# Optimization experiments

Hardware: AMD Instinct MI355X
Metric: run time of the kernel (lower is better)

Reference implementation:

```python
import jax, jax.numpy as jnp
import numpy as np

B, P = 16, 1024
D_TIME, NUM_MODS = 8, 22
DIM_S = NUM_MODS + D_TIME + 1  # 31
PHI_W, N_HEADS, DP = 32, 4, 32
PSI_W, PSI_L, RHO_W = 64, 64, 64
SQRT_DP = float(np.sqrt(DP))


def setup_inputs() -> dict:
    key = jax.random.key(0)
    ks = jax.random.split(key, 16)
    rn = lambda k, shape: jax.random.normal(k, shape, jnp.float32) * 0.05
    return dict(
        times=jax.random.uniform(ks[0], (B, P), jnp.float32) * 48.0,
        values=jax.random.normal(ks[1], (B, P), jnp.float32),
        measurements=jax.random.randint(ks[2], (B, P), 0, NUM_MODS + 1),
        non_pad_mask=jnp.ones((B, P, 1), jnp.float32),
        W_psi1=rn(ks[3], (DIM_S, PSI_W)), b_psi1=jnp.zeros((PSI_W,), jnp.float32),
        W_psi2=rn(ks[4], (PSI_W, PSI_L)), b_psi2=jnp.zeros((PSI_L,), jnp.float32),
        W_key=rn(ks[5], (DIM_S + PSI_L, N_HEADS * DP)), b_key=jnp.zeros((N_HEADS * DP,), jnp.float32),
        query=rn(ks[6], (N_HEADS, DP)),
        W_phi1=rn(ks[7], (DIM_S, PHI_W)), b_phi1=jnp.zeros((PHI_W,), jnp.float32),
        W_phi2=rn(ks[8], (PHI_W, PHI_W)), b_phi2=jnp.zeros((PHI_W,), jnp.float32),
        W_rho1=rn(ks[9], (N_HEADS * PHI_W, RHO_W)), b_rho1=jnp.zeros((RHO_W,), jnp.float32),
        W_rho2=rn(ks[10], (RHO_W, RHO_W)), b_rho2=jnp.zeros((RHO_W,), jnp.float32),
    )


def _temporal_enc(times):
    i = np.arange(D_TIME)
    pos_vec = jnp.asarray(10000.0 ** (2.0 * (i // 2) / D_TIME), jnp.float32)
    ang = times[:, :, None] / pos_vec  # [B,P,d_time]
    return jnp.where(jnp.asarray(i % 2 == 0), jnp.sin(ang), jnp.cos(ang))


def reference(times, values, measurements, non_pad_mask,
              W_psi1, b_psi1, W_psi2, b_psi2, W_key, b_key, query,
              W_phi1, b_phi1, W_phi2, b_phi2, W_rho1, b_rho1, W_rho2, b_rho2):
    m = non_pad_mask  # [B,P,1]
    te = _temporal_enc(times)
    oh = jax.nn.one_hot(measurements, NUM_MODS + 1, dtype=jnp.float32)[:, :, 1:]
    x = jnp.concatenate([te, values[:, :, None], oh], axis=-1)  # [B,P,dim_s]

    # CumulativeSetAttentionLayer: psi MLP -> cumulative mean -> keys . query
    psi = jax.nn.relu(jax.nn.relu(x @ W_psi1 + b_psi1) @ W_psi2 + b_psi2)  # [B,P,psi_l]
    cum = jnp.cumsum(psi * m, axis=1) / jnp.cumsum(m, axis=1)
    keys = (jnp.concatenate([x, cum], axis=-1) @ W_key + b_key).reshape(B, P, N_HEADS, DP)
    pre = jnp.einsum('bpmd,md->bpm', keys, query) / SQRT_DP  # [B,P,m]

    # phi MLP
    phi = jax.nn.relu(jax.nn.relu(x @ W_phi1 + b_phi1) @ W_phi2 + b_phi2) * m  # [B,P,phi_w]

    # cumulative softmax weighting (online path)
    cmax = jax.lax.cummax(pre, axis=1)  # [B,P,m], running max for stability
    D = jnp.exp(pre[:, None, :, :] - cmax[:, :, None, :])  # [B,P,Q,m]
    causal = jnp.arange(P)[:, None] >= jnp.arange(P)[None, :]  # keep Q <= P
    D = D * causal[None, :, :, None]
    E = D.sum(axis=2)  # [B,P,m]
    agg = jnp.einsum('bpqm,bqd->bpmd', D, phi) / E[:, :, :, None]
    agg = (agg * m[:, :, :, None]).reshape(B, P, N_HEADS * PHI_W)

    # rho MLP (return_sequences)
    out = jax.nn.relu(jax.nn.relu(agg @ W_rho1 + b_rho1) @ W_rho2 + b_rho2) * m
    return out
```

## Files before the change

### kernel.cpp

```cpp
#include <hip/hip_runtime.h>
#include <hip/hip_bf16.h>

#define B_ 16
#define P_ 1024
#define T_ (B_*P_)
#define CH_ 32
#define CL_ (P_/CH_)

constexpr int OFF_A     = 16;
constexpr int OFF_WPSI1 = 400;
constexpr int OFF_BPSI1 = OFF_WPSI1 + 1984;
constexpr int OFF_WPSI2 = OFF_BPSI1 + 64;
constexpr int OFF_BPSI2 = OFF_WPSI2 + 4096;
constexpr int OFF_WPHI1 = OFF_BPSI2 + 64;
constexpr int OFF_BPHI1 = OFF_WPHI1 + 992;
constexpr int OFF_WPHI2 = OFF_BPHI1 + 32;
constexpr int OFF_BPHI2 = OFF_WPHI2 + 1024;
constexpr int OFF_WRHO1 = OFF_BPHI2 + 32;
constexpr int OFF_BRHO1 = OFF_WRHO1 + 8192;
constexpr int OFF_WRHO2 = OFF_BRHO1 + 64;
constexpr int OFF_BRHO2 = OFF_WRHO2 + 4096;
constexpr int OFF_PHI   = OFF_BRHO2 + 64;
constexpr int OFF_Z     = OFF_PHI   + T_*32;
constexpr int OFF_PREX  = OFF_Z     + T_*4;
constexpr int OFF_EXPW  = OFF_PREX  + T_*4;
constexpr int OFF_CE    = OFF_EXPW  + T_*4;
constexpr int OFF_CS    = OFF_CE    + 2048;

static __device__ __forceinline__ bool detect_f32(const void* mask_raw) {
  return ((*(const unsigned*)mask_raw) & 0xFFFFu) == 0u;
}
static __device__ __forceinline__ float ld_any(const void* src, int i, bool isf32) {
  if (isf32) return ((const float*)src)[i];
  return __bfloat162float(((const __hip_bfloat16*)src)[i]);
}
static __device__ __forceinline__ float bfbits(unsigned u) {
  union { unsigned q; float f; } x; x.q = u << 16; return x.f;
}

__global__ __launch_bounds__(256) void s01_prep(
    float* __restrict__ ws, const void* mask,
    const void* Wpsi1, const void* bpsi1, const void* Wpsi2, const void* bpsi2,
    const void* Wkey,  const void* bkey,  const void* query,
    const void* Wphi1, const void* bphi1, const void* Wphi2, const void* bphi2) {
  const bool isf32 = detect_f32(mask);
  if (blockIdx.x < 2) {
    const int gid = blockIdx.x * 256 + threadIdx.x;
    if (gid >= 384) return;
    const float inv_s = 0.17677669529663687f;
    const int h = gid & 3;
    const int j = gid >> 2;
    float s = 0.f;
    if (j < 95) {
      for (int d = 0; d < 32; ++d)
        s += ld_any(Wkey, j * 128 + h * 32 + d, isf32) * ld_any(query, h * 32 + d, isf32);
    } else {
      for (int d = 0; d < 32; ++d)
        s += ld_any(bkey, h * 32 + d, isf32) * ld_any(query, h * 32 + d, isf32);
    }
    ws[OFF_A + gid] = s * inv_s;
    return;
  }
  const int g  = (blockIdx.x - 2) * 256 + threadIdx.x;
  const int gs = (gridDim.x - 2) * 256;
  auto st = [&](int off, const void* src, int n) {
    for (int i = g; i < n; i += gs) ws[off + i] = ld_any(src, i, isf32);
  };
  st(OFF_WPSI1, Wpsi1, 1984); st(OFF_BPSI1, bpsi1, 64);
  st(OFF_WPSI2, Wpsi2, 4096); st(OFF_BPSI2, bpsi2, 64);
  st(OFF_WPHI1, Wphi1, 992);  st(OFF_BPHI1, bphi1, 32);
  st(OFF_WPHI2, Wphi2, 1024); st(OFF_BPHI2, bphi2, 32);
}

__global__ __launch_bounds__(1024) void k1_token(float* __restrict__ ws,
                                                 const int* __restrict__ measp,
                                                 const void* __restrict__ times,
                                                 const void* __restrict__ values,
                                                 const void* __restrict__ mask) {
  __shared__ float sWS[8288];
  __shared__ float sh1[32][64];
  __shared__ float sg1[32][32];
  constexpr int LW1 = 0, LB1 = 1984, LW2 = 2048, LB2 = 6144;
  constexpr int LP1 = 6208, LQ1 = 7200, LP2 = 7232, LQ2 = 8256;
  const bool isf32 = detect_f32(mask);
  const int tid = threadIdx.x;
  const int wv  = __builtin_amdgcn_readfirstlane(tid >> 6);
  const int j   = tid & 63;
  const int ta  = blockIdx.x * 32 + wv * 2;
  const int tb  = ta + 1;

  const float tva = ld_any(times, ta, isf32),  tvb = ld_any(times, tb, isf32);
  const float vva = ld_any(values, ta, isf32), vvb = ld_any(values, tb, isf32);
  const float mva = ld_any(mask, ta, isf32),   mvb = ld_any(mask, tb, isf32);
  const int   mea = measp[ta],                 meb = measp[tb];

  {
    const float4* src = (const float4*)(ws + OFF_WPSI1);
    float4* dst = (float4*)sWS;
    for (int i = tid; i < 2072; i += 1024) dst[i] = src[i];
  }

  const float sea = (mea > 0) ? 1.f : 0.f;
  const float seb = (meb > 0) ? 1.f : 0.f;
  const int   mra = (mea > 0) ? (8 + mea) : 0;
  const int   mrb = (meb > 0) ? (8 + meb) : 0;

  float xa[9], xb[9];
  const float posv[4] = {1.f, 10.f, 100.f, 1000.f};
  #pragma unroll
  for (int k = 0; k < 4; ++k) {
    float s, c;
    __sincosf(tva / posv[k], &s, &c); xa[2*k] = s; xa[2*k+1] = c;
    __sincosf(tvb / posv[k], &s, &c); xb[2*k] = s; xb[2*k+1] = c;
  }
  xa[8] = vva; xb[8] = vvb;
  __syncthreads();

  float h1a = sWS[LB1 + j], h1b = h1a;
  #pragma unroll
  for (int i = 0; i < 9; ++i) {
    const float w = sWS[LW1 + i * 64 + j];
    h1a = fmaf(xa[i], w, h1a);
    h1b = fmaf(xb[i], w, h1b);
  }
  h1a = fmaf(sea, sWS[LW1 + mra * 64 + j], h1a);
  h1b = fmaf(seb, sWS[LW1 + mrb * 64 + j], h1b);
  sh1[wv * 2 + 0][j] = fmaxf(h1a, 0.f);
  sh1[wv * 2 + 1][j] = fmaxf(h1b, 0.f);

  if (j < 32) {
    float g1a = sWS[LQ1 + j], g1b = g1a;
    #pragma unroll
    for (int i = 0; i < 9; ++i) {
      const float w = sWS[LP1 + i * 32 + j];
      g1a = fmaf(xa[i], w, g1a);
      g1b = fmaf(xb[i], w, g1b);
    }
    g1a = fmaf(sea, sWS[LP1 + mra * 32 + j], g1a);
    g1b = fmaf(seb, sWS[LP1 + mrb * 32 + j], g1b);
    sg1[wv * 2 + 0][j] = fmaxf(g1a, 0.f);
    sg1[wv * 2 + 1][j] = fmaxf(g1b, 0.f);
  }
  __syncthreads();

  float h2a = sWS[LB2 + j], h2b = h2a;
  #pragma unroll 8
  for (int i = 0; i < 64; ++i) {
    const float w = sWS[LW2 + i * 64 + j];
    h2a = fmaf(sh1[wv * 2 + 0][i], w, h2a);
    h2b = fmaf(sh1[wv * 2 + 1][i], w, h2b);
  }
  const float qa = fmaxf(h2a, 0.f) * mva;
  const float qb = fmaxf(h2b, 0.f) * mvb;

  const float4 a2 = *(const float4*)(ws + OFF_A + (31 + j) * 4);
  float z0a = qa * a2.x, z1a = qa * a2.y, z2a = qa * a2.z, z3a = qa * a2.w;
  float z0b = qb * a2.x, z1b = qb * a2.y, z2b = qb * a2.z, z3b = qb * a2.w;
  #pragma unroll
  for (int off = 32; off; off >>= 1) {
    z0a += __shfl_xor(z0a, off, 64); z1a += __shfl_xor(z1a, off, 64);
    z2a += __shfl_xor(z2a, off, 64); z3a += __shfl_xor(z3a, off, 64);
    z0b += __shfl_xor(z0b, off, 64); z1b += __shfl_xor(z1b, off, 64);
    z2b += __shfl_xor(z2b, off, 64); z3b += __shfl_xor(z3b, off, 64);
  }
  if (j == 0) {
    float4 va; va.x = z0a; va.y = z1a; va.z = z2a; va.w = z3a;
    float4 vb; vb.x = z0b; vb.y = z1b; vb.z = z2b; vb.w = z3b;
    *(float4*)(ws + OFF_Z + (size_t)ta * 4) = va;
    *(float4*)(ws + OFF_Z + (size_t)tb * 4) = vb;
  }

  if (j < 32) {
    float g2a = sWS[LQ2 + j], g2b = g2a;
    #pragma unroll 8
    for (int i = 0; i < 32; ++i) {
      const float w = sWS[LP2 + i * 32 + j];
      g2a = fmaf(sg1[wv * 2 + 0][i], w, g2a);
      g2b = fmaf(sg1[wv * 2 + 1][i], w, g2b);
    }
    ws[OFF_PHI + (size_t)ta * 32 + j] = fmaxf(g2a, 0.f) * mva;
    ws[OFF_PHI + (size_t)tb * 32 + j] = fmaxf(g2b, 0.f) * mvb;
  } else if (j < 40) {
    const bool sec = j >= 36;
    const int h = (j - 32) & 3;
    const float sel  = sec ? seb : sea;
    const int   mrow = sec ? mrb : mra;
    const int   t    = sec ? tb : ta;
    float pr = ws[OFF_A + 380 + h];
    #pragma unroll
    for (int i = 0; i < 9; ++i) {
      const float xi = sec ? xb[i] : xa[i];
      pr = fmaf(xi, ws[OFF_A + i * 4 + h], pr);
    }
    pr = fmaf(sel, ws[OFF_A + mrow * 4 + h], pr);
    ws[OFF_PREX + (size_t)t * 4 + h] = pr;
  }
}

__global__ __launch_bounds__(256) void k2_scanz(float* __restrict__ ws,
                                                const void* __restrict__ mask) {
  const int b    = blockIdx.x;
  const int tid  = threadIdx.x;
  const int lane = tid & 63;
  const int wv   = tid >> 6;
  const bool isf32 = detect_f32(mask);
  __shared__ float swt[4][5];
  __shared__ float smx[4][4];

  const float* zB = ws + OFF_Z + (size_t)b * P_ * 4;
  const int p0 = tid * 4;

  float lc[4], l0[4], l1[4], l2[4], l3[4];
  float c = 0.f, z0 = 0.f, z1 = 0.f, z2 = 0.f, z3 = 0.f;
  const float4* z4 = (const float4*)(zB + (size_t)p0 * 4);
  #pragma unroll
  for (int i = 0; i < 4; ++i) {
    const float4 zv = z4[i];
    c  += ld_any(mask, b * P_ + p0 + i, isf32);
    z0 += zv.x; z1 += zv.y; z2 += zv.z; z3 += zv.w;
    lc[i] = c; l0[i] = z0; l1[i] = z1; l2[i] = z2; l3[i] = z3;
  }

  float rc = c, r0 = z0, r1 = z1, r2 = z2, r3 = z3;
  #pragma unroll
  for (int off = 1; off < 64; off <<= 1) {
    const float uc = __shfl_up(rc, off, 64);
    const float u0 = __shfl_up(r0, off, 64);
    const float u1 = __shfl_up(r1, off, 64);
    const float u2 = __shfl_up(r2, off, 64);
    const float u3 = __shfl_up(r3, off, 64);
    if (lane >= off) { rc += uc; r0 += u0; r1 += u1; r2 += u2; r3 += u3; }
  }
  if (lane == 63) {
    swt[wv][0] = rc; swt[wv][1] = r0; swt[wv][2] = r1; swt[wv][3] = r2; swt[wv][4] = r3;
  }
  __syncthreads();
  #pragma unroll
  for (int w2 = 0; w2 < 3; ++w2) {
    if (wv > w2) {
      rc += swt[w2][0]; r0 += swt[w2][1]; r1 += swt[w2][2];
      r2 += swt[w2][3]; r3 += swt[w2][4];
    }
  }
  const float ec = rc - c, e0 = r0 - z0, e1 = r1 - z1, e2 = r2 - z2, e3 = r3 - z3;

  const float* px = ws + OFF_PREX + (size_t)b * P_ * 4;
  const float4* px4 = (const float4*)(px + (size_t)p0 * 4);
  float pre[4][4];
  float mx0 = -1e30f, mx1 = -1e30f, mx2 = -1e30f, mx3 = -1e30f;
  #pragma unroll
  for (int i = 0; i < 4; ++i) {
    const float inv = 1.f / (ec + lc[i]);
    const float4 pv = px4[i];
    pre[i][0] = pv.x + (e0 + l0[i]) * inv;
    pre[i][1] = pv.y + (e1 + l1[i]) * inv;
    pre[i][2] = pv.z + (e2 + l2[i]) * inv;
    pre[i][3] = pv.w + (e3 + l3[i]) * inv;
    mx0 = fmaxf(mx0, pre[i][0]); mx1 = fmaxf(mx1, pre[i][1]);
    mx2 = fmaxf(mx2, pre[i][2]); mx3 = fmaxf(mx3, pre[i][3]);
  }

  #pragma unroll
  for (int off = 32; off; off >>= 1) {
    mx0 = fmaxf(mx0, __shfl_xor(mx0, off, 64));
    mx1 = fmaxf(mx1, __shfl_xor(mx1, off, 64));
    mx2 = fmaxf(mx2, __shfl_xor(mx2, off, 64));
    mx3 = fmaxf(mx3, __shfl_xor(mx3, off, 64));
  }
  if (lane == 0) { smx[wv][0] = mx0; smx[wv][1] = mx1; smx[wv][2] = mx2; smx[wv][3] = mx3; }
  __syncthreads();
  const float M0 = fmaxf(fmaxf(smx[0][0], smx[1][0]), fmaxf(smx[2][0], smx[3][0]));
  const float M1 = fmaxf(fmaxf(smx[0][1], smx[1][1]), fmaxf(smx[2][1], smx[3][1]));
  const float M2 = fmaxf(fmaxf(smx[0][2], smx[1][2]), fmaxf(smx[2][2], smx[3][2]));
  const float M3 = fmaxf(fmaxf(smx[0][3], smx[1][3]), fmaxf(smx[2][3], smx[3][3]));

  float* eB = ws + OFF_EXPW + (size_t)b * P_ * 4;
  float4* e4 = (float4*)(eB + (size_t)p0 * 4);
  #pragma unroll
  for (int i = 0; i < 4; ++i) {
    float4 ev;
    ev.x = __expf(pre[i][0] - M0);
    ev.y = __expf(pre[i][1] - M1);
    ev.z = __expf(pre[i][2] - M2);
    ev.w = __expf(pre[i][3] - M3);
    e4[i] = ev;
  }
}

__global__ __launch_bounds__(128) void k4a_sums(float* __restrict__ ws) {
  const int ch = blockIdx.x, b = blockIdx.y;
  const int h = threadIdx.x >> 5, d = threadIdx.x & 31;
  const float* eB   = ws + OFF_EXPW + (size_t)b * P_ * 4;
  const float* phiB = ws + OFF_PHI  + (size_t)b * P_ * 32;

  float E = 0.f, S = 0.f;
  const int pbeg = ch * CL_;
  #pragma unroll 4
  for (int p = pbeg; p < pbeg + CL_; ++p) {
    const float e  = eB[p * 4 + h];
    const float ph = phiB[p * 32 + d];
    E += e;
    S = fmaf(e, ph, S);
  }
  const int base = (b * CH_ + ch) * 4 + h;
  if (d == 0) ws[OFF_CE + base] = E;
  ws[OFF_CS + base * 32 + d] = S;
}

__global__ __launch_bounds__(256) void k45_fused(float* __restrict__ ws,
    const void* __restrict__ mask,
    const void* __restrict__ Wrho1, const void* __restrict__ brho1,
    const void* __restrict__ Wrho2, const void* __restrict__ brho2,
    void* __restrict__ out) {
  __shared__ float sW1[8192];
  __shared__ float sAgg[32][128];
  __shared__ float sH1[32][64];
  __shared__ float sEloc[32][4];
  __shared__ float sPreS[128];
  __shared__ float sPreE[4];
  const int ch = blockIdx.x, b = blockIdx.y;
  const int tid = threadIdx.x;
  const bool isf32 = detect_f32(mask);
  const int pbeg = ch * CL_;

  if (tid < 128) {
    const int h = tid >> 5, d = tid & 31;
    const float* eB   = ws + OFF_EXPW + (size_t)b * P_ * 4;
    const float* phiB = ws + OFF_PHI  + (size_t)b * P_ * 32;
    float E = 0.f, S = 0.f;
    #pragma unroll 4
    for (int p = pbeg; p < pbeg + CL_; ++p) {
      const float e  = eB[p * 4 + h];
      const float ph = phiB[p * 32 + d];
      E += e;
      S = fmaf(e, ph, S);
      sAgg[p - pbeg][h * 32 + d] = S;
      if (d == 0) sEloc[p - pbeg][h] = E;
    }
  } else {
    const int tt = tid - 128;
    if (isf32) {
      const float4* w1 = (const float4*)Wrho1;
      for (int i = tt; i < 2048; i += 128) {
        const float4 v = w1[i];
        float* dst = sW1 + i * 4;
        dst[0] = v.x; dst[1] = v.y; dst[2] = v.z; dst[3] = v.w;
      }
    } else {
      const uint4* w1 = (const uint4*)Wrho1;
      for (int i = tt; i < 1024; i += 128) {
        const uint4 v = w1[i];
        float* dst = sW1 + i * 8;
        dst[0] = bfbits(v.x & 0xFFFFu); dst[1] = bfbits(v.x >> 16);
        dst[2] = bfbits(v.y & 0xFFFFu); dst[3] = bfbits(v.y >> 16);
        dst[4] = bfbits(v.z & 0xFFFFu); dst[5] = bfbits(v.z >> 16);
        dst[6] = bfbits(v.w & 0xFFFFu); dst[7] = bfbits(v.w >> 16);
      }
    }
    const int h = tt >> 5, d = tt & 31;
    float E0 = 0.f, S0 = 0.f;
    #pragma unroll 4
    for (int c2 = 0; c2 < ch; ++c2) {
      const int base2 = (b * CH_ + c2) * 4 + h;
      E0 += ws[OFF_CE + base2];
      S0 += ws[OFF_CS + base2 * 32 + d];
    }
    sPreS[tt] = S0;
    if (d == 0) sPreE[h] = E0;
  }
  __syncthreads();

  #pragma unroll
  for (int k = 0; k < 16; ++k) {
    const int slot = tid + k * 256;
    const int p = slot >> 7, c = slot & 127, h2 = c >> 5;
    const float Et = sPreE[h2] + sEloc[p][h2];
    const float St = sPreS[c] + sAgg[p][c];
    sAgg[p][c] = (St / Et) * ld_any(mask, b * P_ + pbeg + p, isf32);
  }
  __syncthreads();

  const int j = tid & 63, qw = tid >> 6;
  const float b1 = ld_any(brho1, j, isf32);
  float acc[8];
  #pragma unroll
  for (int k = 0; k < 8; ++k) acc[k] = b1;
  for (int i4 = 0; i4 < 32; ++i4) {
    const float w0 = sW1[(i4 * 4 + 0) * 64 + j];
    const float w1 = sW1[(i4 * 4 + 1) * 64 + j];
    const float w2 = sW1[(i4 * 4 + 2) * 64 + j];
    const float w3 = sW1[(i4 * 4 + 3) * 64 + j];
    #pragma unroll
    for (int k = 0; k < 8; ++k) {
      const float4 a = *(const float4*)&sAgg[qw * 8 + k][i4 * 4];
      acc[k] = fmaf(a.w, w3, fmaf(a.z, w2, fmaf(a.y, w1, fmaf(a.x, w0, acc[k]))));
    }
  }
  #pragma unroll
  for (int k = 0; k < 8; ++k) sH1[qw * 8 + k][j] = fmaxf(acc[k], 0.f);
  __syncthreads();

  const float b2 = ld_any(brho2, j, isf32);
  float o[8];
  #pragma unroll
  for (int k = 0; k < 8; ++k) o[k] = b2;
  if (isf32) {
    const float* W2 = (const float*)Wrho2;
    #pragma unroll 4
    for (int i = 0; i < 64; ++i) {
      const float w = W2[i * 64 + j];
      #pragma unroll
      for (int k = 0; k < 8; ++k) o[k] = fmaf(sH1[qw * 8 + k][i], w, o[k]);
    }
  } else {
    const __hip_bfloat16* W2 = (const __hip_bfloat16*)Wrho2;
    #pragma unroll 4
    for (int i = 0; i < 64; ++i) {
      const float w = __bfloat162float(W2[i * 64 + j]);
      #pragma unroll
      for (int k = 0; k < 8; ++k) o[k] = fmaf(sH1[qw * 8 + k][i], w, o[k]);
    }
  }

  const int t0 = b * P_ + pbeg + qw * 8;
  #pragma unroll
  for (int k = 0; k < 8; ++k) {
    const float mv = ld_any(mask, t0 + k, isf32);
    const float v  = fmaxf(o[k], 0.f) * mv;
    if (isf32) {
      ((float*)out)[(size_t)(t0 + k) * 64 + j] = v;
    } else {
      ((__hip_bfloat16*)out)[(size_t)(t0 + k) * 64 + j] = __float2bfloat16(v);
    }
  }
}

extern "C" void kernel_launch(void* const* d_in, const int* in_sizes, int n_in,
                              void* d_out, int out_size, void* d_ws, size_t ws_size,
                              hipStream_t stream) {
  const int* meas = (const int*)d_in[2];
  const void* times = d_in[0];
  const void* values = d_in[1];
  const void* mask = d_in[3];
  float* ws = (float*)d_ws;

  s01_prep<<<10, 256, 0, stream>>>(ws, mask,
                                   d_in[4], d_in[5], d_in[6], d_in[7],
                                   d_in[8], d_in[9], d_in[10],
                                   d_in[11], d_in[12], d_in[13], d_in[14]);
  k1_token<<<T_/32, 1024, 0, stream>>>(ws, meas, times, values, mask);
  k2_scanz<<<B_, 256, 0, stream>>>(ws, mask);
  k4a_sums<<<dim3(CH_, B_), 128, 0, stream>>>(ws);
  k45_fused<<<dim3(CH_, B_), 256, 0, stream>>>(ws, mask,
                                               d_in[15], d_in[16], d_in[17], d_in[18],
                                               d_out);
}
```

Before: 142.0 us.

## Fuse z-scan and chunk sums into chunked scan with per-chunk softmax max rescaling

Replaces the per-batch serial scan kernel (16 blocks) and the separate chunk-sum kernel with one chunk-parallel kernel over (32 chunks x 16 batches). k1_token now emits per-32-token chunk totals of mask and z so each chunk can compute its prefix locally. Each chunk uses its own local max for the exponentials, and k45_fused rescales the earlier chunk sums to a common running max. This removes a kernel launch and the low-parallelism scan, at the cost of extra exp work and a somewhat different numerical-stability scheme.

```diff
diff --git a/kernel.cpp b/kernel.cpp
--- a/kernel.cpp
+++ b/kernel.cpp
@@ -26,6 +26,8 @@
 constexpr int OFF_EXPW  = OFF_PREX  + T_*4;
 constexpr int OFF_CE    = OFF_EXPW  + T_*4;
 constexpr int OFF_CS    = OFF_CE    + 2048;
+constexpr int OFF_CZ    = OFF_CS    + 65536;
+constexpr int OFF_CM    = OFF_CZ    + 4096;
 
 static __device__ __forceinline__ bool detect_f32(const void* mask_raw) {
   return ((*(const unsigned*)mask_raw) & 0xFFFFu) == 0u;
@@ -80,6 +82,7 @@
   __shared__ float sWS[8288];
   __shared__ float sh1[32][64];
   __shared__ float sg1[32][32];
+  __shared__ float swz[16][5];
   constexpr int LW1 = 0, LB1 = 1984, LW2 = 2048, LB2 = 6144;
   constexpr int LP1 = 6208, LQ1 = 7200, LP2 = 7232, LQ2 = 8256;
   const bool isf32 = detect_f32(mask);
@@ -168,6 +171,9 @@
     float4 vb; vb.x = z0b; vb.y = z1b; vb.z = z2b; vb.w = z3b;
     *(float4*)(ws + OFF_Z + (size_t)ta * 4) = va;
     *(float4*)(ws + OFF_Z + (size_t)tb * 4) = vb;
+    swz[wv][0] = mva + mvb;
+    swz[wv][1] = z0a + z0b; swz[wv][2] = z1a + z1b;
+    swz[wv][3] = z2a + z2b; swz[wv][4] = z3a + z3b;
   }
 
   if (j < 32) {
@@ -195,112 +201,86 @@
     pr = fmaf(sel, ws[OFF_A + mrow * 4 + h], pr);
     ws[OFF_PREX + (size_t)t * 4 + h] = pr;
   }
-}
-
-__global__ __launch_bounds__(256) void k2_scanz(float* __restrict__ ws,
+
+  __syncthreads();
+  if (tid < 5) {
+    float s = 0.f;
+    #pragma unroll
+    for (int w = 0; w < 16; ++w) s += swz[w][tid];
+    ws[OFF_CZ + (size_t)blockIdx.x * 8 + tid] = s;
+  }
+}
+
+__global__ __launch_bounds__(128) void k2b_scan(float* __restrict__ ws,
                                                 const void* __restrict__ mask) {
-  const int b    = blockIdx.x;
-  const int tid  = threadIdx.x;
-  const int lane = tid & 63;
-  const int wv   = tid >> 6;
+  const int ch = blockIdx.x, b = blockIdx.y;
+  const int tid = threadIdx.x;
   const bool isf32 = detect_f32(mask);
-  __shared__ float swt[4][5];
-  __shared__ float smx[4][4];
-
-  const float* zB = ws + OFF_Z + (size_t)b * P_ * 4;
-  const int p0 = tid * 4;
-
-  float lc[4], l0[4], l1[4], l2[4], l3[4];
-  float c = 0.f, z0 = 0.f, z1 = 0.f, z2 = 0.f, z3 = 0.f;
-  const float4* z4 = (const float4*)(zB + (size_t)p0 * 4);
-  #pragma unroll
-  for (int i = 0; i < 4; ++i) {
-    const float4 zv = z4[i];
-    c  += ld_any(mask, b * P_ + p0 + i, isf32);
-    z0 += zv.x; z1 += zv.y; z2 += zv.z; z3 += zv.w;
-    lc[i] = c; l0[i] = z0; l1[i] = z1; l2[i] = z2; l3[i] = z3;
-  }
-
-  float rc = c, r0 = z0, r1 = z1, r2 = z2, r3 = z3;
-  #pragma unroll
-  for (int off = 1; off < 64; off <<= 1) {
-    const float uc = __shfl_up(rc, off, 64);
-    const float u0 = __shfl_up(r0, off, 64);
-    const float u1 = __shfl_up(r1, off, 64);
-    const float u2 = __shfl_up(r2, off, 64);
-    const float u3 = __shfl_up(r3, off, 64);
-    if (lane >= off) { rc += uc; r0 += u0; r1 += u1; r2 += u2; r3 += u3; }
-  }
-  if (lane == 63) {
-    swt[wv][0] = rc; swt[wv][1] = r0; swt[wv][2] = r1; swt[wv][3] = r2; swt[wv][4] = r3;
-  }
-  __syncthreads();
-  #pragma unroll
-  for (int w2 = 0; w2 < 3; ++w2) {
-    if (wv > w2) {
-      rc += swt[w2][0]; r0 += swt[w2][1]; r1 += swt[w2][2];
-      r2 += swt[w2][3]; r3 += swt[w2][4];
-    }
-  }
-  const float ec = rc - c, e0 = r0 - z0, e1 = r1 - z1, e2 = r2 - z2, e3 = r3 - z3;
-
-  const float* px = ws + OFF_PREX + (size_t)b * P_ * 4;
-  const float4* px4 = (const float4*)(px + (size_t)p0 * 4);
-  float pre[4][4];
-  float mx0 = -1e30f, mx1 = -1e30f, mx2 = -1e30f, mx3 = -1e30f;
-  #pragma unroll
-  for (int i = 0; i < 4; ++i) {
-    const float inv = 1.f / (ec + lc[i]);
-    const float4 pv = px4[i];
-    pre[i][0] = pv.x + (e0 + l0[i]) * inv;
-    pre[i][1] = pv.y + (e1 + l1[i]) * inv;
-    pre[i][2] = pv.z + (e2 + l2[i]) * inv;
-    pre[i][3] = pv.w + (e3 + l3[i]) * inv;
-    mx0 = fmaxf(mx0, pre[i][0]); mx1 = fmaxf(mx1, pre[i][1]);
-    mx2 = fmaxf(mx2, pre[i][2]); mx3 = fmaxf(mx3, pre[i][3]);
-  }
-
-  #pragma unroll
-  for (int off = 32; off; off >>= 1) {
-    mx0 = fmaxf(mx0, __shfl_xor(mx0, off, 64));
-    mx1 = fmaxf(mx1, __shfl_xor(mx1, off, 64));
-    mx2 = fmaxf(mx2, __shfl_xor(mx2, off, 64));
-    mx3 = fmaxf(mx3, __shfl_xor(mx3, off, 64));
-  }
-  if (lane == 0) { smx[wv][0] = mx0; smx[wv][1] = mx1; smx[wv][2] = mx2; smx[wv][3] = mx3; }
-  __syncthreads();
-  const float M0 = fmaxf(fmaxf(smx[0][0], smx[1][0]), fmaxf(smx[2][0], smx[3][0]));
-  const float M1 = fmaxf(fmaxf(smx[0][1], smx[1][1]), fmaxf(smx[2][1], smx[3][1]));
-  const float M2 = fmaxf(fmaxf(smx[0][2], smx[1][2]), fmaxf(smx[2][2], smx[3][2]));
-  const float M3 = fmaxf(fmaxf(smx[0][3], smx[1][3]), fmaxf(smx[2][3], smx[3][3]));
-
-  float* eB = ws + OFF_EXPW + (size_t)b * P_ * 4;
-  float4* e4 = (float4*)(eB + (size_t)p0 * 4);
-  #pragma unroll
-  for (int i = 0; i < 4; ++i) {
+  __shared__ float sE[32][4];
+  const int pbeg = ch * CL_;
+
+  if (tid < 32) {
+    const int p = tid;
+    float pc = 0.f, p0 = 0.f, p1 = 0.f, p2 = 0.f, p3 = 0.f;
+    if (p < ch) {
+      const float* cz = ws + OFF_CZ + (size_t)(b * CH_ + p) * 8;
+      pc = cz[0]; p0 = cz[1]; p1 = cz[2]; p2 = cz[3]; p3 = cz[4];
+    }
+    #pragma unroll
+    for (int mm = 16; mm; mm >>= 1) {
+      pc += __shfl_xor(pc, mm, 32);
+      p0 += __shfl_xor(p0, mm, 32);
+      p1 += __shfl_xor(p1, mm, 32);
+      p2 += __shfl_xor(p2, mm, 32);
+      p3 += __shfl_xor(p3, mm, 32);
+    }
+    const int tglob = b * P_ + pbeg + p;
+    float c = ld_any(mask, tglob, isf32);
+    const float4 zv = *(const float4*)(ws + OFF_Z + (size_t)tglob * 4);
+    float z0 = zv.x, z1 = zv.y, z2 = zv.z, z3 = zv.w;
+    #pragma unroll
+    for (int off = 1; off < 32; off <<= 1) {
+      const float uc = __shfl_up(c,  off, 32);
+      const float u0 = __shfl_up(z0, off, 32);
+      const float u1 = __shfl_up(z1, off, 32);
+      const float u2 = __shfl_up(z2, off, 32);
+      const float u3 = __shfl_up(z3, off, 32);
+      if (p >= off) { c += uc; z0 += u0; z1 += u1; z2 += u2; z3 += u3; }
+    }
+    const float inv = 1.f / (pc + c);
+    const float4 pxv = *(const float4*)(ws + OFF_PREX + (size_t)tglob * 4);
+    const float pr0 = pxv.x + (p0 + z0) * inv;
+    const float pr1 = pxv.y + (p1 + z1) * inv;
+    const float pr2 = pxv.z + (p2 + z2) * inv;
+    const float pr3 = pxv.w + (p3 + z3) * inv;
+    float m0 = pr0, m1 = pr1, m2 = pr2, m3 = pr3;
+    #pragma unroll
+    for (int mm = 16; mm; mm >>= 1) {
+      m0 = fmaxf(m0, __shfl_xor(m0, mm, 32));
+      m1 = fmaxf(m1, __shfl_xor(m1, mm, 32));
+      m2 = fmaxf(m2, __shfl_xor(m2, mm, 32));
+      m3 = fmaxf(m3, __shfl_xor(m3, mm, 32));
+    }
     float4 ev;
-    ev.x = __expf(pre[i][0] - M0);
-    ev.y = __expf(pre[i][1] - M1);
-    ev.z = __expf(pre[i][2] - M2);
-    ev.w = __expf(pre[i][3] - M3);
-    e4[i] = ev;
-  }
-}
-
-__global__ __launch_bounds__(128) void k4a_sums(float* __restrict__ ws) {
-  const int ch = blockIdx.x, b = blockIdx.y;
-  const int h = threadIdx.x >> 5, d = threadIdx.x & 31;
-  const float* eB   = ws + OFF_EXPW + (size_t)b * P_ * 4;
-  const float* phiB = ws + OFF_PHI  + (size_t)b * P_ * 32;
-
+    ev.x = __expf(pr0 - m0); ev.y = __expf(pr1 - m1);
+    ev.z = __expf(pr2 - m2); ev.w = __expf(pr3 - m3);
+    *(float4*)(ws + OFF_EXPW + (size_t)tglob * 4) = ev;
+    sE[p][0] = ev.x; sE[p][1] = ev.y; sE[p][2] = ev.z; sE[p][3] = ev.w;
+    if (p == 0) {
+      float* cm = ws + OFF_CM + (size_t)(b * CH_ + ch) * 4;
+      cm[0] = m0; cm[1] = m1; cm[2] = m2; cm[3] = m3;
+    }
+  }
+  __syncthreads();
+
+  const int h = tid >> 5, d = tid & 31;
+  const float* phiB = ws + OFF_PHI + (size_t)b * P_ * 32 + (size_t)pbeg * 32;
   float E = 0.f, S = 0.f;
-  const int pbeg = ch * CL_;
   #pragma unroll 4
-  for (int p = pbeg; p < pbeg + CL_; ++p) {
-    const float e  = eB[p * 4 + h];
-    const float ph = phiB[p * 32 + d];
+  for (int p = 0; p < 32; ++p) {
+    const float e = sE[p][h];
     E += e;
-    S = fmaf(e, ph, S);
+    S = fmaf(e, phiB[p * 32 + d], S);
   }
   const int base = (b * CH_ + ch) * 4 + h;
   if (d == 0) ws[OFF_CE + base] = E;
@@ -318,6 +298,7 @@
   __shared__ float sEloc[32][4];
   __shared__ float sPreS[128];
   __shared__ float sPreE[4];
+  __shared__ float sFo[4];
   const int ch = blockIdx.x, b = blockIdx.y;
   const int tid = threadIdx.x;
   const bool isf32 = detect_f32(mask);
@@ -358,15 +339,19 @@
       }
     }
     const int h = tt >> 5, d = tt & 31;
+    const float* cmB = ws + OFF_CM + (size_t)b * CH_ * 4;
+    const float Mown = cmB[ch * 4 + h];
+    float Mst = Mown;
+    for (int c2 = 0; c2 < ch; ++c2) Mst = fmaxf(Mst, cmB[c2 * 4 + h]);
     float E0 = 0.f, S0 = 0.f;
-    #pragma unroll 4
     for (int c2 = 0; c2 < ch; ++c2) {
+      const float f = __expf(cmB[c2 * 4 + h] - Mst);
       const int base2 = (b * CH_ + c2) * 4 + h;
-      E0 += ws[OFF_CE + base2];
-      S0 += ws[OFF_CS + base2 * 32 + d];
+      E0 = fmaf(ws[OFF_CE + base2], f, E0);
+      S0 = fmaf(ws[OFF_CS + base2 * 32 + d], f, S0);
     }
     sPreS[tt] = S0;
-    if (d == 0) sPreE[h] = E0;
+    if (d == 0) { sPreE[h] = E0; sFo[h] = __expf(Mown - Mst); }
   }
   __syncthreads();
 
@@ -374,8 +359,9 @@
   for (int k = 0; k < 16; ++k) {
     const int slot = tid + k * 256;
     const int p = slot >> 7, c = slot & 127, h2 = c >> 5;
-    const float Et = sPreE[h2] + sEloc[p][h2];
-    const float St = sPreS[c] + sAgg[p][c];
+    const float fo = sFo[h2];
+    const float Et = sPreE[h2] + fo * sEloc[p][h2];
+    const float St = sPreS[c] + fo * sAgg[p][c];
     sAgg[p][c] = (St / Et) * ld_any(mask, b * P_ + pbeg + p, isf32);
   }
   __syncthreads();
@@ -449,8 +435,7 @@
                                    d_in[8], d_in[9], d_in[10],
                                    d_in[11], d_in[12], d_in[13], d_in[14]);
   k1_token<<<T_/32, 1024, 0, stream>>>(ws, meas, times, values, mask);
-  k2_scanz<<<B_, 256, 0, stream>>>(ws, mask);
-  k4a_sums<<<dim3(CH_, B_), 128, 0, stream>>>(ws);
+  k2b_scan<<<dim3(CH_, B_), 128, 0, stream>>>(ws, mask);
   k45_fused<<<dim3(CH_, B_), 256, 0, stream>>>(ws, mask,
                                                d_in[15], d_in[16], d_in[17], d_in[18],
                                                d_out);
```

After: 145.4 us. 2.4% more time.
